# Kernel tuning notes

Measured on AMD Instinct MI355X. Metric: run time of the kernel, lower is better.

Reference implementation:

```python
import jax, jax.numpy as jnp
import numpy as np

DELTA_T = 0.25
K_SUB = int(round(1.0 / DELTA_T))  # Euler substeps per observation (unit-spaced times)


def setup_inputs() -> dict:
    key = jax.random.key(0)
    ks = jax.random.split(key, 16)
    B, T, IN, XH, G, HID, OUT = 512, 128, 128, 512, 256, 256, 128
    s = 0.05
    inp = {
        "H": jax.random.normal(ks[0], (B, T, IN), jnp.float32),
        "times": jnp.arange(T, dtype=jnp.int64 if jax.config.jax_enable_x64 else jnp.int32).reshape(1, T),
        # x_model: Linear(IN,XH) -> ReLU -> Linear(XH,G); stored as [in,out]
        "W1": jax.random.normal(ks[1], (IN, XH), jnp.float32) * s,
        "b1": jax.random.normal(ks[2], (XH,), jnp.float32) * s,
        "W2": jax.random.normal(ks[3], (XH, G), jnp.float32) * s,
        "b2": jax.random.normal(ks[4], (G,), jnp.float32) * s,
        # FullGRUODECell_Autonomous: three bias-free [HID,HID] linears (torch [out,in])
        "Ohr": jax.random.normal(ks[5], (HID, HID), jnp.float32) * s,
        "Ohz": jax.random.normal(ks[6], (HID, HID), jnp.float32) * s,
        "Ohh": jax.random.normal(ks[7], (HID, HID), jnp.float32) * s,
        # torch.nn.GRU(G, HID): weights [3H, in], gate order r,z,n
        "Wih": jax.random.normal(ks[8], (3 * HID, G), jnp.float32) * s,
        "Whh": jax.random.normal(ks[9], (3 * HID, HID), jnp.float32) * s,
        "bih": jax.random.normal(ks[10], (3 * HID,), jnp.float32) * s,
        "bhh": jax.random.normal(ks[11], (3 * HID,), jnp.float32) * s,
        # rec_linear: Linear(G, OUT), stored as [in,out]
        "Wr": jax.random.normal(ks[12], (G, OUT), jnp.float32) * s,
        "br": jax.random.normal(ks[13], (OUT,), jnp.float32) * s,
    }
    return inp


def _forward(H, W1, b1, W2, b2, Ohr, Ohz, Ohh, Wih, Whh, bih, bhh, Wr, br):
    # x_model
    HH = jnp.maximum(H @ W1 + b1, 0.0) @ W2 + b2  # [B, T, G]
    B = HH.shape[0]
    HID = Ohr.shape[0]

    # GRU-ODE Euler substep (autonomous cell: input is implicitly zero)
    def ode_substep(h, _):
        r = jax.nn.sigmoid(h @ Ohr.T)
        z = jax.nn.sigmoid(h @ Ohz.T)
        u = jnp.tanh((r * h) @ Ohh.T)
        return h + DELTA_T * ((1.0 - z) * (u - h)), None

    Wir, Wiz, Win = jnp.split(Wih, 3, axis=0)
    Uhr, Uhz, Uhn = jnp.split(Whh, 3, axis=0)
    bir, biz, bin_ = jnp.split(bih, 3)
    bhr, bhz, bhn = jnp.split(bhh, 3)

    def step(h, x_t):  # x_t: [B, G]
        h, _ = jax.lax.scan(ode_substep, h, None, length=K_SUB)
        r = jax.nn.sigmoid(x_t @ Wir.T + bir + h @ Uhr.T + bhr)
        z = jax.nn.sigmoid(x_t @ Wiz.T + biz + h @ Uhz.T + bhz)
        n = jnp.tanh(x_t @ Win.T + bin_ + r * (h @ Uhn.T + bhn))
        h_new = (1.0 - z) * n + z * h  # GRU output for one step == new hidden
        return h_new, h_new

    h0 = jnp.zeros((B, HID), HH.dtype)
    _, outs = jax.lax.scan(step, h0, jnp.swapaxes(HH, 0, 1))  # [T, B, HID]
    out = jnp.swapaxes(outs, 0, 1)  # [B, T, HID] (== gru_input_size)
    return out @ Wr + br  # identity last activation


def reference(H, times, W1, b1, W2, b2, Ohr, Ohz, Ohh, Wih, Whh, bih, bhh, Wr, br):
    # times are unit-spaced (arange); the data-dependent while-loop of the
    # original reduces to exactly K_SUB Euler substeps before each observation.
    return _forward(H, W1, b1, W2, b2, Ohr, Ohz, Ohh, Wih, Whh, bih, bhh, Wr, br)
```

## Files before the change

### kernel.cpp

```cpp
#include <hip/hip_runtime.h>

typedef unsigned short ushort;
typedef unsigned int uint;
typedef __bf16 bf16x8 __attribute__((ext_vector_type(8)));
typedef ushort ushort8 __attribute__((ext_vector_type(8)));
typedef float f32x4 __attribute__((ext_vector_type(4)));

#define Z4 f32x4{0.f, 0.f, 0.f, 0.f}

__device__ __forceinline__ f32x4 mfma16(bf16x8 a, bf16x8 b, f32x4 c) {
    return __builtin_amdgcn_mfma_f32_16x16x32_bf16(a, b, c, 0, 0, 0);
}
__device__ __forceinline__ float bf2f(ushort h) {
    union { uint u; float f; } v; v.u = ((uint)h) << 16; return v.f;
}
__device__ __forceinline__ ushort f2bf(float f) {
    union { float f; uint u; } v; v.f = f;
    uint u = v.u;
    uint r = (u + 0x7fffu + ((u >> 16) & 1u)) >> 16;
    return (ushort)r;
}
__device__ __forceinline__ float sigmoidf_(float x) { return 1.f / (1.f + __expf(-x)); }
__device__ __forceinline__ float tanhf_(float x) {
    float e = __expf(2.f * x);
    return 1.f - 2.f / (e + 1.f);
}

typedef __attribute__((address_space(1))) uint guint;
typedef __attribute__((address_space(3))) uint luint;
__device__ __forceinline__ void dma16(const ushort* g, ushort* l) {
    __builtin_amdgcn_global_load_lds((const guint*)g, (luint*)l, 16, 0, 0);
}
template <int N> __device__ __forceinline__ void ring_wait() {
    asm volatile("s_waitcnt vmcnt(%0)" ::"n"(N) : "memory");
}
__device__ __forceinline__ void wg_sync() {
    asm volatile("s_waitcnt lgkmcnt(0)\n\ts_barrier" ::: "memory");
}

__global__ void pack_direct_k(const float* __restrict__ src, ushort* __restrict__ dst,
                              int N, int K) {
    int total = (N >> 4) * (K >> 5) * 64;
    int idx = blockIdx.x * 256 + threadIdx.x;
    if (idx >= total) return;
    int l = idx & 63, f = idx >> 6;
    int kfrags = K >> 5;
    int nt = f / kfrags, kf = f - nt * kfrags;
    int n = nt * 16 + (l & 15);
    int k0 = kf * 32 + (l >> 4) * 8;
    const float* s = src + (size_t)n * K + k0;
    ushort8 u;
#pragma unroll
    for (int j = 0; j < 8; j++) u[j] = f2bf(s[j]);
    *(ushort8*)&dst[(size_t)f * 512 + l * 8] = u;
}
__global__ void pack_trans_k(const float* __restrict__ src, ushort* __restrict__ dst,
                             int N, int K) {
    int total = (N >> 4) * (K >> 5) * 64;
    int idx = blockIdx.x * 256 + threadIdx.x;
    if (idx >= total) return;
    int l = idx & 63, f = idx >> 6;
    int kfrags = K >> 5;
    int nt = f / kfrags, kf = f - nt * kfrags;
    int n = nt * 16 + (l & 15);
    int k0 = kf * 32 + (l >> 4) * 8;
    ushort8 u;
#pragma unroll
    for (int j = 0; j < 8; j++) u[j] = f2bf(src[(size_t)(k0 + j) * N + n]);
    *(ushort8*)&dst[(size_t)f * 512 + l * 8] = u;
}

__global__ __launch_bounds__(256) void mlp_kernel(
    const float* __restrict__ H,
    const ushort* __restrict__ W1P,
    const float* __restrict__ b1,
    const ushort* __restrict__ W2P,
    const float* __restrict__ b2,
    ushort* __restrict__ X2)
{
    __shared__ __align__(16) ushort sH[64][136];
    __shared__ __align__(16) ushort sT[64][264];
    __shared__ float sb1[512], sb2[256];
    const int tid = threadIdx.x;
    const int w = tid >> 6, lane = tid & 63;
    const int q = lane >> 4, tc = lane & 15;
    const int lo8 = lane * 8;
    const int m0 = blockIdx.x * 64;

    {
        int r = tid >> 2, c0 = (tid & 3) * 32;
        const float* src = H + (size_t)(m0 + r) * 128 + c0;
#pragma unroll
        for (int v = 0; v < 4; v++) {
            float4 a = *(const float4*)(src + v * 8);
            float4 b = *(const float4*)(src + v * 8 + 4);
            ushort8 u;
            u[0] = f2bf(a.x); u[1] = f2bf(a.y); u[2] = f2bf(a.z); u[3] = f2bf(a.w);
            u[4] = f2bf(b.x); u[5] = f2bf(b.y); u[6] = f2bf(b.z); u[7] = f2bf(b.w);
            *(ushort8*)&sH[r][c0 + v * 8] = u;
        }
    }
    for (int i = tid; i < 512; i += 256) sb1[i] = b1[i];
    if (tid < 256) sb2[tid] = b2[tid];
    __syncthreads();

    bf16x8 af[4];
#pragma unroll
    for (int kb = 0; kb < 4; kb++) af[kb] = *(const bf16x8*)&sH[w * 16 + tc][kb * 32 + q * 8];

    f32x4 accH[16];
#pragma unroll
    for (int nt = 0; nt < 16; nt++) accH[nt] = Z4;

#pragma unroll 1
    for (int half = 0; half < 2; half++) {
        __syncthreads();
#pragma unroll
        for (int j = 0; j < 16; j++) {
            int n = half * 256 + j * 16 + tc;
            const ushort* bp = W1P + (size_t)((half * 16 + j) * 4) * 512 + lo8;
            f32x4 a = Z4;
#pragma unroll
            for (int kb = 0; kb < 4; kb++)
                a = mfma16(af[kb], *(const bf16x8*)(bp + kb * 512), a);
            float bv = sb1[n];
#pragma unroll
            for (int i = 0; i < 4; i++)
                sT[w * 16 + q * 4 + i][j * 16 + tc] = f2bf(fmaxf(a[i] + bv, 0.f));
        }
        __syncthreads();

        bf16x8 a2[8];
#pragma unroll
        for (int kb = 0; kb < 8; kb++) a2[kb] = *(const bf16x8*)&sT[w * 16 + tc][kb * 32 + q * 8];
#pragma unroll
        for (int nt = 0; nt < 16; nt++) {
            const ushort* bp = W2P + (size_t)(nt * 16 + half * 8) * 512 + lo8;
#pragma unroll
            for (int kb = 0; kb < 8; kb++)
                accH[nt] = mfma16(a2[kb], *(const bf16x8*)(bp + kb * 512), accH[nt]);
        }
    }

#pragma unroll
    for (int nt = 0; nt < 16; nt++) {
        int col = nt * 16 + tc;
        float bv = sb2[col];
#pragma unroll
        for (int i = 0; i < 4; i++)
            X2[(size_t)(m0 + w * 16 + q * 4 + i) * 256 + col] = f2bf(accH[nt][i] + bv);
    }
}

__global__ __launch_bounds__(256) void gemm128P(
    const ushort* __restrict__ A, const ushort* __restrict__ BP,
    const float* __restrict__ bias, void* __restrict__ Cout,
    int M, int N, int K, int mode)
{
    __shared__ __align__(16) ushort sA[128][40];
    const int tid = threadIdx.x;
    const int lane = tid & 63, wid = tid >> 6;
    const int q = lane >> 4, tc = lane & 15;
    const int lo8 = lane * 8;
    const int wm = (wid >> 1) * 64, wn = (wid & 1) * 64;
    const int bm = blockIdx.y * 128, bn = blockIdx.x * 128;

    f32x4 acc[4][4];
#pragma unroll
    for (int im = 0; im < 4; im++)
#pragma unroll
        for (int in_ = 0; in_ < 4; in_++) acc[im][in_] = Z4;

    const int arow = tid >> 1, acol = (tid & 1) * 16;
    const int kfrags = K >> 5;

    for (int kc = 0; kc < K; kc += 32) {
        const ushort* ga = A + (size_t)(bm + arow) * K + kc + acol;
        ushort8 va0 = *(const ushort8*)ga;
        ushort8 va1 = *(const ushort8*)(ga + 8);
        __syncthreads();
        *(ushort8*)&sA[arow][acol] = va0;
        *(ushort8*)&sA[arow][acol + 8] = va1;
        __syncthreads();

        bf16x8 af[4], bf[4];
#pragma unroll
        for (int im = 0; im < 4; im++) af[im] = *(const bf16x8*)&sA[wm + im * 16 + tc][q * 8];
#pragma unroll
        for (int in_ = 0; in_ < 4; in_++) {
            int nt = ((bn + wn) >> 4) + in_;
            bf[in_] = *(const bf16x8*)(BP + (size_t)(nt * kfrags + (kc >> 5)) * 512 + lo8);
        }
#pragma unroll
        for (int im = 0; im < 4; im++)
#pragma unroll
            for (int in_ = 0; in_ < 4; in_++)
                acc[im][in_] = mfma16(af[im], bf[in_], acc[im][in_]);
    }

#pragma unroll
    for (int in_ = 0; in_ < 4; in_++) {
        int col = bn + wn + in_ * 16 + tc;
        float bv = bias[col];
#pragma unroll
        for (int im = 0; im < 4; im++) {
            int row0 = bm + wm + im * 16 + q * 4;
#pragma unroll
            for (int r = 0; r < 4; r++) {
                float v = acc[im][in_][r] + bv;
                int row = row0 + r;
                if (mode == 0) {
                    ((ushort*)Cout)[(size_t)row * N + col] = f2bf(v);
                } else if (mode == 1) {
                    ((float*)Cout)[(size_t)row * N + col] = v;
                } else {
                    int b = row >> 7, t = row & 127;
                    size_t dst = (((size_t)(b >> 4) * 128 + t) * N + col) * 16 + (b & 15);
                    ((ushort*)Cout)[dst] = f2bf(v);
                }
            }
        }
    }
}

__global__ __launch_bounds__(1024) void scan_fused(
    const ushort* __restrict__ XgSw,
    const ushort* __restrict__ OhrP, const ushort* __restrict__ OhzP,
    const ushort* __restrict__ OhhP,
    const ushort* __restrict__ WhhP,
    const float*  __restrict__ bhh,
    ushort* __restrict__ hseq)
{
    const int bx = blockIdx.x;
    const int m0 = bx * 16;
    const int tid = threadIdx.x;
    const int w = tid >> 6, lane = tid & 63;
    const int q = lane >> 4, tc = lane & 15;
    const int lo8 = lane * 8;
    const int colbase = w * 16 + tc;

    __shared__ __align__(16) ushort ring[16][3][1024];
    __shared__ __align__(16) ushort h_bf[16][264];
    __shared__ __align__(16) ushort rh_bf[16][264];

    for (int i = tid; i < 16 * 264; i += 1024) (&h_bf[0][0])[i] = 0;

    float rbv = bhh[colbase], zbv = bhh[256 + colbase], hnbv = bhh[512 + colbase];

    bf16x8 wOr[8], wOz[8];
#pragma unroll
    for (int f = 0; f < 8; f++) {
        wOr[f] = *(const bf16x8*)(OhrP + (size_t)(w * 8 + f) * 512 + lo8);
        wOz[f] = *(const bf16x8*)(OhzP + (size_t)(w * 8 + f) * 512 + lo8);
    }

    float hreg[4] = {0.f, 0.f, 0.f, 0.f};

    int ic = 0, islot = 0, slot = 0;
    auto pump = [&]() {
        if (ic >= 28) return;
        asm volatile("s_waitcnt lgkmcnt(0)" ::: "memory");
        const ushort* g;
        if (ic < 16) {
            g = OhhP + (size_t)(w * 8 + (ic & 3) * 2) * 512;
        } else {
            int j = ic - 16, gg = j % 3, kc = j / 3;
            g = WhhP + (size_t)((gg * 16 + w) * 8 + kc * 2) * 512;
        }
        g += lo8;
        ushort* sb = &ring[w][islot][0];
        dma16(g, sb); dma16(g + 512, sb + 512);
        ic++; islot = (islot == 2) ? 0 : islot + 1;
    };

    __syncthreads();

#pragma unroll 1
    for (int t = 0; t < 128; t++) {
        const ushort* xgp = XgSw + (((size_t)bx * 128 + t) * 768) * 16;
        uint2 xg[3];
#pragma unroll
        for (int g = 0; g < 3; g++)
            xg[g] = *(const uint2*)(xgp + (size_t)(g * 256 + colbase) * 16 + q * 4);

        ic = 0; islot = 0; slot = 0;
        pump(); pump(); pump();

#pragma unroll 1
        for (int s = 0; s < 4; s++) {
            f32x4 ar = Z4, az = Z4;
#pragma unroll
            for (int kh = 0; kh < 2; kh++) {
                bf16x8 af[4];
#pragma unroll
                for (int k = 0; k < 4; k++)
                    af[k] = *(const bf16x8*)&h_bf[tc][(kh * 4 + k) * 32 + q * 8];
#pragma unroll
                for (int k = 0; k < 4; k++) {
                    ar = mfma16(af[k], wOr[kh * 4 + k], ar);
                    az = mfma16(af[k], wOz[kh * 4 + k], az);
                }
            }
#pragma unroll
            for (int i = 0; i < 4; i++)
                rh_bf[q * 4 + i][colbase] = f2bf(sigmoidf_(ar[i]) * hreg[i]);
            wg_sync();

            f32x4 uu = Z4;
#pragma unroll
            for (int cc = 0; cc < 4; cc++) {
                bf16x8 au0 = *(const bf16x8*)&rh_bf[tc][(cc * 2) * 32 + q * 8];
                bf16x8 au1 = *(const bf16x8*)&rh_bf[tc][(cc * 2 + 1) * 32 + q * 8];
                ring_wait<4>();
                const ushort* sb = &ring[w][slot][0] + lo8;
                bf16x8 v0 = *(const bf16x8*)(sb);
                bf16x8 v1 = *(const bf16x8*)(sb + 512);
                slot = (slot == 2) ? 0 : slot + 1;
                pump();
                uu = mfma16(au0, v0, uu);
                uu = mfma16(au1, v1, uu);
            }
#pragma unroll
            for (int i = 0; i < 4; i++) {
                float zv = sigmoidf_(az[i]);
                float hv = hreg[i];
                float hn = hv + 0.25f * (1.f - zv) * (tanhf_(uu[i]) - hv);
                hreg[i] = hn;
                h_bf[q * 4 + i][colbase] = f2bf(hn);
            }
            wg_sync();
        }

        f32x4 accr = Z4, accz = Z4, accn = Z4;
#define GRU_CHUNK(J, WN)                                                       \
        {                                                                      \
            constexpr int g_ = (J) % 3, kc_ = (J) / 3;                         \
            bf16x8 ah0 = *(const bf16x8*)&h_bf[tc][(kc_ * 2) * 32 + q * 8];    \
            bf16x8 ah1 = *(const bf16x8*)&h_bf[tc][(kc_ * 2 + 1) * 32 + q * 8];\
            ring_wait<WN>();                                                   \
            const ushort* sb = &ring[w][slot][0] + lo8;                        \
            bf16x8 v0 = *(const bf16x8*)(sb);                                  \
            bf16x8 v1 = *(const bf16x8*)(sb + 512);                            \
            slot = (slot == 2) ? 0 : slot + 1;                                 \
            pump();                                                            \
            f32x4* tg = (g_ == 0) ? &accr : (g_ == 1) ? &accz : &accn;         \
            *tg = mfma16(ah0, v0, *tg);                                        \
            *tg = mfma16(ah1, v1, *tg);                                        \
        }
        GRU_CHUNK(0, 4)  GRU_CHUNK(1, 4)  GRU_CHUNK(2, 4)  GRU_CHUNK(3, 4)
        GRU_CHUNK(4, 4)  GRU_CHUNK(5, 4)  GRU_CHUNK(6, 4)  GRU_CHUNK(7, 4)
        GRU_CHUNK(8, 4)  GRU_CHUNK(9, 4)  GRU_CHUNK(10, 2) GRU_CHUNK(11, 0)
#undef GRU_CHUNK
        wg_sync();

        {
            uint2 ur = xg[0], uz = xg[1], un = xg[2];
#pragma unroll
            for (int i = 0; i < 4; i++) {
                int sh = (i & 1) * 16;
                uint wr = (i < 2) ? ur.x : ur.y, wz = (i < 2) ? uz.x : uz.y,
                     wn = (i < 2) ? un.x : un.y;
                float xr = bf2f((ushort)(wr >> sh)), xz = bf2f((ushort)(wz >> sh)),
                      xn = bf2f((ushort)(wn >> sh));
                float rg = sigmoidf_(accr[i] + xr + rbv);
                float zg = sigmoidf_(accz[i] + xz + zbv);
                float ng = tanhf_(xn + rg * (accn[i] + hnbv));
                float hv = hreg[i];
                float hn = (1.f - zg) * ng + zg * hv;
                hreg[i] = hn;
                h_bf[q * 4 + i][colbase] = f2bf(hn);
            }
        }
        wg_sync();

        {
            int row = tid >> 6, col = (tid & 63) * 4;
            *(uint2*)&hseq[((size_t)(m0 + row) * 128 + t) * 256 + col] =
                *(const uint2*)&h_bf[row][col];
        }
    }
}

extern "C" void kernel_launch(void* const* d_in, const int* in_sizes, int n_in,
                              void* d_out, int out_size, void* d_ws, size_t ws_size,
                              hipStream_t stream) {
    const float* H   = (const float*)d_in[0];
    const float* W1  = (const float*)d_in[2];
    const float* b1  = (const float*)d_in[3];
    const float* W2  = (const float*)d_in[4];
    const float* b2  = (const float*)d_in[5];
    const float* Ohr = (const float*)d_in[6];
    const float* Ohz = (const float*)d_in[7];
    const float* Ohh = (const float*)d_in[8];
    const float* Wih = (const float*)d_in[9];
    const float* Whh = (const float*)d_in[10];
    const float* bih = (const float*)d_in[11];
    const float* bhh = (const float*)d_in[12];
    const float* Wr  = (const float*)d_in[13];
    const float* br  = (const float*)d_in[14];
    float* out = (float*)d_out;
    char* ws = (char*)d_ws;

    ushort* Xg   = (ushort*)(ws);
    ushort* X2   = (ushort*)(ws + 100663296);
    ushort* hseq = X2;
    char* pk = ws + 134217728;
    ushort* W1P  = (ushort*)(pk);
    ushort* W2P  = (ushort*)(pk + 131072);
    ushort* WrP  = (ushort*)(pk + 393216);
    ushort* OhrP = (ushort*)(pk + 458752);
    ushort* OhzP = (ushort*)(pk + 589824);
    ushort* OhhP = (ushort*)(pk + 720896);
    ushort* WihP = (ushort*)(pk + 851968);

    pack_trans_k<<<dim3(32),  256, 0, stream>>>(W1,  W1P, 512, 128);
    pack_trans_k<<<dim3(64),  256, 0, stream>>>(W2,  W2P, 256, 512);
    pack_trans_k<<<dim3(16),  256, 0, stream>>>(Wr,  WrP, 128, 256);
    pack_direct_k<<<dim3(32), 256, 0, stream>>>(Ohr, OhrP, 256, 256);
    pack_direct_k<<<dim3(32), 256, 0, stream>>>(Ohz, OhzP, 256, 256);
    pack_direct_k<<<dim3(32), 256, 0, stream>>>(Ohh, OhhP, 256, 256);
    pack_direct_k<<<dim3(96), 256, 0, stream>>>(Wih, WihP, 768, 256);
    pack_direct_k<<<dim3(96), 256, 0, stream>>>(Whh, (ushort*)(pk + 1245184), 768, 256);
    ushort* WhhP = (ushort*)(pk + 1245184);

    mlp_kernel<<<dim3(1024), 256, 0, stream>>>(H, W1P, b1, W2P, b2, X2);
    gemm128P<<<dim3(6, 512), 256, 0, stream>>>(X2, WihP, bih, Xg, 65536, 768, 256, 2);

    scan_fused<<<dim3(32), 1024, 0, stream>>>(Xg, OhrP, OhzP, OhhP, WhhP, bhh, hseq);

    gemm128P<<<dim3(1, 512), 256, 0, stream>>>(hseq, WrP, br, out, 65536, 128, 256, 1);
}
```

Baseline: 2.772 ms.

## Split scan batch rows across twice as many workgroups using half-filled MFMA tiles

The recurrent scan kernel now handles 8 batch rows per workgroup instead of 16, launching 64 workgroups instead of 32 so more compute units work through the serial time loop. MFMA tiles stay 16 rows tall. Rows 8-15 of h_bf and rh_bf stay zero as padding, and lane shuffles redistribute accumulator results so each lane owns two real rows. This trades half of the MFMA throughput per workgroup, plus twice the total weight streaming through the LDS ring, for shorter per-step elementwise work and more parallelism across the chip.

```diff
diff --git a/kernel.cpp b/kernel.cpp
--- a/kernel.cpp
+++ b/kernel.cpp
@@ -232,18 +232,21 @@
     ushort* __restrict__ hseq)
 {
     const int bx = blockIdx.x;
-    const int m0 = bx * 16;
+    const int m0 = bx * 8;
     const int tid = threadIdx.x;
     const int w = tid >> 6, lane = tid & 63;
     const int q = lane >> 4, tc = lane & 15;
     const int lo8 = lane * 8;
     const int colbase = w * 16 + tc;
+    const int R = ((lane >> 4) & 1) * 4 + ((lane >> 5) << 1);
+    const bool lo = (q < 2);
 
     __shared__ __align__(16) ushort ring[16][3][1024];
     __shared__ __align__(16) ushort h_bf[16][264];
     __shared__ __align__(16) ushort rh_bf[16][264];
 
     for (int i = tid; i < 16 * 264; i += 1024) (&h_bf[0][0])[i] = 0;
+    for (int i = tid; i < 16 * 264; i += 1024) (&rh_bf[0][0])[i] = 0;
 
     float rbv = bhh[colbase], zbv = bhh[256 + colbase], hnbv = bhh[512 + colbase];
 
@@ -254,7 +257,7 @@
         wOz[f] = *(const bf16x8*)(OhzP + (size_t)(w * 8 + f) * 512 + lo8);
     }
 
-    float hreg[4] = {0.f, 0.f, 0.f, 0.f};
+    float hreg[2] = {0.f, 0.f};
 
     int ic = 0, islot = 0, slot = 0;
     auto pump = [&]() {
@@ -277,11 +280,12 @@
 
 #pragma unroll 1
     for (int t = 0; t < 128; t++) {
-        const ushort* xgp = XgSw + (((size_t)bx * 128 + t) * 768) * 16;
-        uint2 xg[3];
+        const ushort* xgp = XgSw + (((size_t)(bx >> 1) * 128 + t) * 768) * 16
+                            + (bx & 1) * 8 + R;
+        uint xg[3];
 #pragma unroll
         for (int g = 0; g < 3; g++)
-            xg[g] = *(const uint2*)(xgp + (size_t)(g * 256 + colbase) * 16 + q * 4);
+            xg[g] = *(const uint*)(xgp + (size_t)(g * 256 + colbase) * 16);
 
         ic = 0; islot = 0; slot = 0;
         pump(); pump(); pump();
@@ -301,9 +305,12 @@
                     az = mfma16(af[k], wOz[kh * 4 + k], az);
                 }
             }
-#pragma unroll
-            for (int i = 0; i < 4; i++)
-                rh_bf[q * 4 + i][colbase] = f2bf(sigmoidf_(ar[i]) * hreg[i]);
+            float ar2 = __shfl(ar[2], lane & 31), ar3 = __shfl(ar[3], lane & 31);
+            float az2 = __shfl(az[2], lane & 31), az3 = __shfl(az[3], lane & 31);
+            float ea0 = lo ? ar[0] : ar2, ea1 = lo ? ar[1] : ar3;
+            float ez0 = lo ? az[0] : az2, ez1 = lo ? az[1] : az3;
+            rh_bf[R + 0][colbase] = f2bf(sigmoidf_(ea0) * hreg[0]);
+            rh_bf[R + 1][colbase] = f2bf(sigmoidf_(ea1) * hreg[1]);
             wg_sync();
 
             f32x4 uu = Z4;
@@ -320,13 +327,19 @@
                 uu = mfma16(au0, v0, uu);
                 uu = mfma16(au1, v1, uu);
             }
-#pragma unroll
-            for (int i = 0; i < 4; i++) {
-                float zv = sigmoidf_(az[i]);
-                float hv = hreg[i];
-                float hn = hv + 0.25f * (1.f - zv) * (tanhf_(uu[i]) - hv);
-                hreg[i] = hn;
-                h_bf[q * 4 + i][colbase] = f2bf(hn);
+            float uu2 = __shfl(uu[2], lane & 31), uu3 = __shfl(uu[3], lane & 31);
+            float eu0 = lo ? uu[0] : uu2, eu1 = lo ? uu[1] : uu3;
+            {
+                float zv = sigmoidf_(ez0), hv = hreg[0];
+                float hn = hv + 0.25f * (1.f - zv) * (tanhf_(eu0) - hv);
+                hreg[0] = hn;
+                h_bf[R + 0][colbase] = f2bf(hn);
+            }
+            {
+                float zv = sigmoidf_(ez1), hv = hreg[1];
+                float hn = hv + 0.25f * (1.f - zv) * (tanhf_(eu1) - hv);
+                hreg[1] = hn;
+                h_bf[R + 1][colbase] = f2bf(hn);
             }
             wg_sync();
         }
@@ -354,29 +367,41 @@
         wg_sync();
 
         {
-            uint2 ur = xg[0], uz = xg[1], un = xg[2];
-#pragma unroll
-            for (int i = 0; i < 4; i++) {
-                int sh = (i & 1) * 16;
-                uint wr = (i < 2) ? ur.x : ur.y, wz = (i < 2) ? uz.x : uz.y,
-                     wn = (i < 2) ? un.x : un.y;
-                float xr = bf2f((ushort)(wr >> sh)), xz = bf2f((ushort)(wz >> sh)),
-                      xn = bf2f((ushort)(wn >> sh));
-                float rg = sigmoidf_(accr[i] + xr + rbv);
-                float zg = sigmoidf_(accz[i] + xz + zbv);
-                float ng = tanhf_(xn + rg * (accn[i] + hnbv));
-                float hv = hreg[i];
+            float r2 = __shfl(accr[2], lane & 31), r3 = __shfl(accr[3], lane & 31);
+            float z2 = __shfl(accz[2], lane & 31), z3 = __shfl(accz[3], lane & 31);
+            float n2 = __shfl(accn[2], lane & 31), n3 = __shfl(accn[3], lane & 31);
+            float er0 = lo ? accr[0] : r2, er1 = lo ? accr[1] : r3;
+            float ez0 = lo ? accz[0] : z2, ez1 = lo ? accz[1] : z3;
+            float en0 = lo ? accn[0] : n2, en1 = lo ? accn[1] : n3;
+            {
+                float xr = bf2f((ushort)(xg[0])), xz = bf2f((ushort)(xg[1])),
+                      xn = bf2f((ushort)(xg[2]));
+                float rg = sigmoidf_(er0 + xr + rbv);
+                float zg = sigmoidf_(ez0 + xz + zbv);
+                float ng = tanhf_(xn + rg * (en0 + hnbv));
+                float hv = hreg[0];
                 float hn = (1.f - zg) * ng + zg * hv;
-                hreg[i] = hn;
-                h_bf[q * 4 + i][colbase] = f2bf(hn);
+                hreg[0] = hn;
+                h_bf[R + 0][colbase] = f2bf(hn);
+            }
+            {
+                float xr = bf2f((ushort)(xg[0] >> 16)), xz = bf2f((ushort)(xg[1] >> 16)),
+                      xn = bf2f((ushort)(xg[2] >> 16));
+                float rg = sigmoidf_(er1 + xr + rbv);
+                float zg = sigmoidf_(ez1 + xz + zbv);
+                float ng = tanhf_(xn + rg * (en1 + hnbv));
+                float hv = hreg[1];
+                float hn = (1.f - zg) * ng + zg * hv;
+                hreg[1] = hn;
+                h_bf[R + 1][colbase] = f2bf(hn);
             }
         }
         wg_sync();
 
         {
-            int row = tid >> 6, col = (tid & 63) * 4;
-            *(uint2*)&hseq[((size_t)(m0 + row) * 128 + t) * 256 + col] =
-                *(const uint2*)&h_bf[row][col];
+            int row = tid >> 7, col = (tid & 127) * 2;
+            *(uint*)&hseq[((size_t)(m0 + row) * 128 + t) * 256 + col] =
+                *(const uint*)&h_bf[row][col];
         }
     }
 }
@@ -426,7 +451,7 @@
     mlp_kernel<<<dim3(1024), 256, 0, stream>>>(H, W1P, b1, W2P, b2, X2);
     gemm128P<<<dim3(6, 512), 256, 0, stream>>>(X2, WihP, bih, Xg, 65536, 768, 256, 2);
 
-    scan_fused<<<dim3(32), 1024, 0, stream>>>(Xg, OhrP, OhzP, OhhP, WhhP, bhh, hseq);
+    scan_fused<<<dim3(64), 1024, 0, stream>>>(Xg, OhrP, OhzP, OhhP, WhhP, bhh, hseq);
 
     gemm128P<<<dim3(1, 512), 256, 0, stream>>>(hseq, WrP, br, out, 65536, 128, 256, 1);
 }
```

New measurement: 2.520 ms. 9.1% less time.
